# Kernel optimization log

Measured on AMD Instinct MI355X. Metric: run time of the kernel, lower is better.

Reference implementation:

```python
import jax, jax.numpy as jnp
import numpy as np


def setup_inputs() -> dict:
    key = jax.random.key(0)
    ks = jax.random.split(key, 7)
    B, P, D = 4, 2048, 1024
    s = 1.0 / np.sqrt(D)
    return {
        "x":  jax.random.normal(ks[0], (B, P, D), dtype=jnp.float32),
        "Wq": jax.random.normal(ks[1], (D, D), dtype=jnp.float32) * s,
        "bq": jnp.zeros((D,), dtype=jnp.float32),
        "Wk": jax.random.normal(ks[2], (D, D), dtype=jnp.float32) * s,
        "bk": jnp.zeros((D,), dtype=jnp.float32),
        "Wv": jax.random.normal(ks[3], (D, D), dtype=jnp.float32) * s,
        "bv": jnp.zeros((D,), dtype=jnp.float32),
    }


def reference(x, Wq, bq, Wk, bk, Wv, bv):
    # x: [B, P, D]; Linear uses W stored torch-style [out, in]: y = x @ W.T + b
    b, p, d = x.shape
    q = jnp.einsum("bpd,ed->bpe", x, Wq) + bq
    k = jnp.einsum("bpd,ed->bpe", x, Wk) + bk
    v = jnp.einsum("bpd,ed->bpe", x, Wv) + bv
    attn = jnp.einsum("bqd,bkd->bqk", q, k)  # [B, P, P]
    causal = jnp.triu(jnp.ones((p, p), dtype=bool), k=1)  # True above diagonal
    attn = jnp.where(causal, -jnp.inf, attn)
    attn = attn / jnp.sqrt(jnp.asarray(d, dtype=attn.dtype))
    scores = jax.nn.softmax(attn, axis=-1)
    # dropout is identity in eval/deterministic mode
    return jnp.einsum("bqk,bkd->bqd", scores, v)
```

## Files before the change

kernel.cpp:

```cpp
#include <hip/hip_runtime.h>
#include <hip/hip_bf16.h>


typedef __attribute__((ext_vector_type(8))) short bf16x8;
typedef __attribute__((ext_vector_type(4))) float f32x4;

__device__ __forceinline__ unsigned short f2bf(float f) {
    union { float f; unsigned u; } v; v.f = f;
    unsigned r = v.u + 0x7FFF + ((v.u >> 16) & 1);
    return (unsigned short)(r >> 16);
}

__device__ __forceinline__ void gload_lds16(const unsigned short* g, unsigned short* l) {
    __builtin_amdgcn_global_load_lds(
        (const __attribute__((address_space(1))) unsigned int*)g,
        (__attribute__((address_space(3))) unsigned int*)l, 16, 0, 0);
}

__global__ void convert_kernel(const float* __restrict__ x,  const float* __restrict__ wq,
                               const float* __restrict__ wk, const float* __restrict__ wv,
                               const float* __restrict__ bq, const float* __restrict__ bk,
                               const float* __restrict__ bv,
                               unsigned short* __restrict__ xb, unsigned short* __restrict__ wqkvb,
                               float* __restrict__ bqkv, float* __restrict__ lsum) {
    long t = (long)blockIdx.x * blockDim.x + threadIdx.x;
    long idx = t * 4;
    const float* src; unsigned short* dst; long off;
    if      (idx <  8388608) { src = x;  dst = xb;            off = idx;            }
    else if (idx <  9437184) { src = wq; dst = wqkvb;         off = idx -  8388608; }
    else if (idx < 10485760) { src = wk; dst = wqkvb+1048576; off = idx -  9437184; }
    else if (idx < 11534336) { src = wv; dst = wqkvb+2097152; off = idx - 10485760; }
    else return;
    float4 v = *(const float4*)(src + off);
    ushort4 o = make_ushort4(f2bf(v.x), f2bf(v.y), f2bf(v.z), f2bf(v.w));
    *(ushort4*)(dst + off) = o;
    if (t < 768) {
        long o2 = t * 4;
        float4 b;
        if      (o2 < 1024) b = *(const float4*)(bq + o2);
        else if (o2 < 2048) b = *(const float4*)(bk + o2 - 1024);
        else                b = *(const float4*)(bv + o2 - 2048);
        *(float4*)(bqkv + o2) = b;
    }
    if (t >= 1024 && t < 3072) {
        float4 z = make_float4(0.f, 0.f, 0.f, 0.f);
        *(float4*)(lsum + (t - 1024) * 4) = z;
    }
}

__device__ __forceinline__ void stage256(const unsigned short* gA, const unsigned short* gB,
                                         unsigned short* lds, int sdst, int t) {
    unsigned short* dst = lds + (t & 3) * 16384;
    const long koff = (long)t * 32;
    gload_lds16(gA + koff,              dst + sdst);
    gload_lds16(gA + koff + 128 * 1024, dst + 4096 + sdst);
    gload_lds16(gB + koff,              dst + 8192 + sdst);
    gload_lds16(gB + koff + 128 * 1024, dst + 12288 + sdst);
}

template<bool SWAP>
__device__ __forceinline__ void qkv256_core(const unsigned short* gA, const unsigned short* gB,
                                            unsigned short* lds, int sdst,
                                            int arow, int brow, int fch,
                                            f32x4 (&acc)[8][4]) {
    stage256(gA, gB, lds, sdst, 0);
    stage256(gA, gB, lds, sdst, 1);
    stage256(gA, gB, lds, sdst, 2);
    asm volatile("s_waitcnt vmcnt(8)" ::: "memory");
    __builtin_amdgcn_s_barrier();
#pragma unroll 1
    for (int t = 0; t < 32; ++t) {
        if (t + 3 < 32) stage256(gA, gB, lds, sdst, t + 3);
        const unsigned short* Ab = lds + (t & 3) * 16384;
        const unsigned short* Bb = Ab + 8192;
        bf16x8 af[8], bf[4];
#pragma unroll
        for (int i = 0; i < 8; ++i)
            af[i] = *(const bf16x8*)(Ab + (arow + i * 16) * 32 + fch);
#pragma unroll
        for (int j = 0; j < 4; ++j)
            bf[j] = *(const bf16x8*)(Bb + (brow + j * 16) * 32 + fch);
        __builtin_amdgcn_s_setprio(1);
#pragma unroll
        for (int i = 0; i < 8; ++i)
#pragma unroll
            for (int j = 0; j < 4; ++j)
                acc[i][j] = SWAP
                    ? __builtin_amdgcn_mfma_f32_16x16x32_bf16(bf[j], af[i], acc[i][j], 0, 0, 0)
                    : __builtin_amdgcn_mfma_f32_16x16x32_bf16(af[i], bf[j], acc[i][j], 0, 0, 0);
        __builtin_amdgcn_s_setprio(0);
        if (t <= 28)      asm volatile("s_waitcnt vmcnt(8)" ::: "memory");
        else if (t == 29) asm volatile("s_waitcnt vmcnt(4)" ::: "memory");
        else if (t == 30) asm volatile("s_waitcnt vmcnt(0)" ::: "memory");
        if (t < 31) __builtin_amdgcn_s_barrier();
    }
}

__global__ __launch_bounds__(512, 2)
void gemm_qkv256(const unsigned short* __restrict__ X,
                 const unsigned short* __restrict__ W,
                 unsigned short* __restrict__ QK,
                 unsigned short* __restrict__ VT,
                 const float* __restrict__ bias) {
    extern __shared__ unsigned short lds[];
    const int n0 = blockIdx.x * 256;
    const int m0 = blockIdx.y * 256;
    const int tid = threadIdx.x, lane = tid & 63, w = tid >> 6;
    const int q = lane >> 4, ln = lane & 15;
    const int wm = w >> 2, wn = w & 3;
    const int srow = tid >> 2;
    const int sch  = (((tid & 3) ^ ((tid >> 3) & 3)) << 3);
    const unsigned short* gA = X + (long)(m0 + srow) * 1024 + sch;
    const unsigned short* gB = W + (long)(n0 + srow) * 1024 + sch;
    const int sdst = tid * 8;
    const int arow = wm * 128 + ln;
    const int brow = wn * 64 + ln;
    const int fch  = ((q ^ ((ln >> 1) & 3)) << 3);
    f32x4 acc[8][4] = {};
    if (n0 >= 2048) {
        qkv256_core<false>(gA, gB, lds, sdst, arow, brow, fch, acc);
#pragma unroll
        for (int j = 0; j < 4; ++j) {
            const int ecol = n0 + wn * 64 + j * 16 + ln;
            const float bc = bias[ecol];
            const int e = ecol - 2048;
#pragma unroll
            for (int i = 0; i < 8; ++i) {
                const int m = m0 + wm * 128 + i * 16 + q * 4;
                ushort4 o = make_ushort4(f2bf(acc[i][j][0] + bc), f2bf(acc[i][j][1] + bc),
                                         f2bf(acc[i][j][2] + bc), f2bf(acc[i][j][3] + bc));
                *(ushort4*)(VT + (long)e * 8192 + m) = o;
            }
        }
    } else {
        qkv256_core<true>(gA, gB, lds, sdst, arow, brow, fch, acc);
#pragma unroll
        for (int j = 0; j < 4; ++j) {
            const float4 bc = *(const float4*)(bias + n0 + wn * 64 + j * 16 + q * 4);
#pragma unroll
            for (int i = 0; i < 8; ++i) {
                const int m = m0 + wm * 128 + i * 16 + ln;
                const int n = n0 + wn * 64 + j * 16 + q * 4;
                ushort4 o = make_ushort4(f2bf(acc[i][j][0] + bc.x), f2bf(acc[i][j][1] + bc.y),
                                         f2bf(acc[i][j][2] + bc.z), f2bf(acc[i][j][3] + bc.w));
                *(ushort4*)(QK + (long)m * 2048 + n) = o;
            }
        }
    }
}

__device__ __forceinline__ void stage(const unsigned short* gA, long lda,
                                      const unsigned short* gB, long ldb,
                                      unsigned short* As, unsigned short* Bs,
                                      int w, int k0) {
#pragma unroll
    for (int s = 0; s < 4; ++s) {
        gload_lds16(gA + k0 + (long)(s * 8) * lda, &As[(w * 32 + s * 8) * 64]);
        gload_lds16(gB + k0 + (long)(s * 8) * ldb, &Bs[(w * 32 + s * 8) * 64]);
    }
}

template<bool SWAP>
__device__ __forceinline__ void mfma_tile(const unsigned short* As, const unsigned short* Bs,
                                          int wr, int wc, int ln, int pr0, int pr1,
                                          f32x4 (&acc)[4][4]) {
#pragma unroll
    for (int kk = 0; kk < 2; ++kk) {
        const int pr = kk ? pr1 : pr0;
        bf16x8 af[4], bfr[4];
#pragma unroll
        for (int i = 0; i < 4; ++i)
            af[i] = *(const bf16x8*)(&As[(wr + i * 16 + ln) * 64 + pr]);
#pragma unroll
        for (int j = 0; j < 4; ++j)
            bfr[j] = *(const bf16x8*)(&Bs[(wc + j * 16 + ln) * 64 + pr]);
#pragma unroll
        for (int i = 0; i < 4; ++i)
#pragma unroll
            for (int j = 0; j < 4; ++j)
                acc[i][j] = SWAP
                    ? __builtin_amdgcn_mfma_f32_16x16x32_bf16(bfr[j], af[i], acc[i][j], 0, 0, 0)
                    : __builtin_amdgcn_mfma_f32_16x16x32_bf16(af[i], bfr[j], acc[i][j], 0, 0, 0);
    }
}

template<bool SWAP>
__device__ __forceinline__ void kloop_db(const unsigned short* gA, long lda,
                                         const unsigned short* gB, long ldb,
                                         unsigned short* As0, unsigned short* Bs0,
                                         unsigned short* As1, unsigned short* Bs1,
                                         int w, int lane, int Keff, f32x4 (&acc)[4][4]) {
    const int q  = lane >> 4;
    const int ln = lane & 15;
    const int wr = (w >> 1) * 64;
    const int wc = (w & 1) * 64;
    const int pr0 = ((q)     ^ (ln & 7)) * 8;
    const int pr1 = ((q + 4) ^ (ln & 7)) * 8;
    stage(gA, lda, gB, ldb, As0, Bs0, w, 0);
    __syncthreads();
    for (int k0 = 0; k0 < Keff; k0 += 128) {
        stage(gA, lda, gB, ldb, As1, Bs1, w, k0 + 64);
        mfma_tile<SWAP>(As0, Bs0, wr, wc, ln, pr0, pr1, acc);
        __syncthreads();
        if (k0 + 128 < Keff)
            stage(gA, lda, gB, ldb, As0, Bs0, w, k0 + 128);
        mfma_tile<SWAP>(As1, Bs1, wr, wc, ln, pr0, pr1, acc);
        __syncthreads();
    }
}

__global__ __launch_bounds__(256, 2)
void gemm_scores(const unsigned short* __restrict__ QK,
                 unsigned short* __restrict__ P,
                 float* __restrict__ lsum) {
    const int t = blockIdx.x;
    int i = (int)((sqrtf(8.0f * t + 1.0f) - 1.0f) * 0.5f);
    while ((i + 1) * (i + 2) / 2 <= t) ++i;
    while (i * (i + 1) / 2 > t) --i;
    const int j = t - i * (i + 1) / 2;
    const int m0 = i * 128, n0 = j * 128, z = blockIdx.y;
    const unsigned short* Qz = QK + (long)z * 2048 * 2048;
    const unsigned short* Kz = Qz + 1024;
    unsigned short* Pz = P + (long)z * 2048 * 2048;
    float* lz = lsum + z * 2048;

    __shared__ __align__(16) unsigned short As0[128 * 64], Bs0[128 * 64];
    __shared__ __align__(16) unsigned short As1[128 * 64], Bs1[128 * 64];
    const int tid = threadIdx.x, lane = tid & 63, w = tid >> 6;
    const int q = lane >> 4, ln = lane & 15;
    const int wr = (w >> 1) * 64, wc = (w & 1) * 64;
    const int srow = lane >> 3, sc = (lane & 7) ^ srow;
    const unsigned short* gA = Qz + (long)(m0 + w * 32 + srow) * 2048 + sc * 8;
    const unsigned short* gB = Kz + (long)(n0 + w * 32 + srow) * 2048 + sc * 8;
    f32x4 acc[4][4] = {};
    kloop_db<true>(gA, 2048, gB, 2048, As0, Bs0, As1, Bs1, w, lane, 1024, acc);

    const float scale = 0.03125f;
#pragma unroll
    for (int i2 = 0; i2 < 4; ++i2) {
        const int m = m0 + wr + i2 * 16 + ln;
        float rs = 0.f;
#pragma unroll
        for (int j2 = 0; j2 < 4; ++j2) {
            const int n = n0 + wc + j2 * 16 + q * 4;
            float p0 = (n     <= m) ? __expf(acc[i2][j2][0] * scale) : 0.f;
            float p1 = (n + 1 <= m) ? __expf(acc[i2][j2][1] * scale) : 0.f;
            float p2 = (n + 2 <= m) ? __expf(acc[i2][j2][2] * scale) : 0.f;
            float p3 = (n + 3 <= m) ? __expf(acc[i2][j2][3] * scale) : 0.f;
            rs += (p0 + p1) + (p2 + p3);
            ushort4 o = make_ushort4(f2bf(p0), f2bf(p1), f2bf(p2), f2bf(p3));
            *(ushort4*)(Pz + (long)m * 2048 + n) = o;
        }
        rs += __shfl_xor(rs, 16); rs += __shfl_xor(rs, 32);
        if (lane < 16) atomicAdd(&lz[m], rs);
    }
}

__global__ __launch_bounds__(256, 2)
void gemm_pv(const unsigned short* __restrict__ P,
             const unsigned short* __restrict__ VT,
             const float* __restrict__ lsum,
             float* __restrict__ out) {
    const int L  = blockIdx.x;
    const int ph = L >> 8;
    const int c  = L & 255;
    const int z  = c >> 6;
    const int r  = c & 63;
    const int mh = r >> 3;
    const int nt = r & 7;
    const int mt = ph ? 15 - mh : mh;
    const int m0 = mt * 128, n0 = nt * 128;
    const int Keff = m0 + 128;
    const unsigned short* Pz = P + (long)z * 2048 * 2048;
    const unsigned short* Vz = VT + (long)z * 2048;
    const float* lz = lsum + z * 2048;

    __shared__ __align__(16) unsigned short As0[128 * 64], Bs0[128 * 64];
    __shared__ __align__(16) unsigned short As1[128 * 64], Bs1[128 * 64];
    const int tid = threadIdx.x, lane = tid & 63, w = tid >> 6;
    const int q = lane >> 4, ln = lane & 15;
    const int wr = (w >> 1) * 64, wc = (w & 1) * 64;
    const int srow = lane >> 3, sc = (lane & 7) ^ srow;
    const unsigned short* gA = Pz + (long)(m0 + w * 32 + srow) * 2048 + sc * 8;
    const unsigned short* gB = Vz + (long)(n0 + w * 32 + srow) * 8192 + sc * 8;
    f32x4 acc[4][4] = {};
    kloop_db<true>(gA, 2048, gB, 8192, As0, Bs0, As1, Bs1, w, lane, Keff, acc);

#pragma unroll
    for (int i2 = 0; i2 < 4; ++i2) {
        const int m = m0 + wr + i2 * 16 + ln;
        const float inv = 1.0f / lz[m];
#pragma unroll
        for (int j2 = 0; j2 < 4; ++j2) {
            const int n = n0 + wc + j2 * 16 + q * 4;
            float4 o = make_float4(acc[i2][j2][0] * inv, acc[i2][j2][1] * inv,
                                   acc[i2][j2][2] * inv, acc[i2][j2][3] * inv);
            *(float4*)(out + (long)(z * 2048 + m) * 1024 + n) = o;
        }
    }
}

extern "C" void kernel_launch(void* const* d_in, const int* in_sizes, int n_in,
                              void* d_out, int out_size, void* d_ws, size_t ws_size,
                              hipStream_t stream) {
    const float* x  = (const float*)d_in[0];
    const float* Wq = (const float*)d_in[1];
    const float* bq = (const float*)d_in[2];
    const float* Wk = (const float*)d_in[3];
    const float* bk = (const float*)d_in[4];
    const float* Wv = (const float*)d_in[5];
    const float* bv = (const float*)d_in[6];
    float* out = (float*)d_out;

    char* ws = (char*)d_ws;
    unsigned short* xb    = (unsigned short*)ws; ws += (long)8192 * 1024 * 2;
    unsigned short* wqkvb = (unsigned short*)ws; ws += (long)3072 * 1024 * 2;
    float*          bqkv  = (float*)ws;          ws += (long)3072 * 4;
    float*          lsum  = (float*)ws;          ws += (long)8192 * 4;
    unsigned short* QKb   = (unsigned short*)ws; ws += (long)8192 * 2048 * 2;
    unsigned short* VTb   = (unsigned short*)ws; ws += (long)1024 * 8192 * 2;
    unsigned short* Pb    = (unsigned short*)ws; ws += (long)4 * 2048 * 2048 * 2;

    hipFuncSetAttribute((const void*)gemm_qkv256,
                        hipFuncAttributeMaxDynamicSharedMemorySize, 131072);

    hipLaunchKernelGGL(convert_kernel, dim3(11264), dim3(256), 0, stream,
                       x, Wq, Wk, Wv, bq, bk, bv, xb, wqkvb, bqkv, lsum);

    hipLaunchKernelGGL(gemm_qkv256, dim3(12, 32, 1), dim3(512), 131072, stream,
                       xb, wqkvb, QKb, VTb, bqkv);

    hipLaunchKernelGGL(gemm_scores, dim3(136, 4, 1), dim3(256), 0, stream,
                       QKb, Pb, lsum);

    hipLaunchKernelGGL(gemm_pv, dim3(512, 1, 1), dim3(256), 0, stream,
                       Pb, VTb, lsum, out);
}
```

Measured before the change: 252.7 us.

## Restructure QKV GEMM main loop into 8-phase interleaved load/MFMA pipeline with BK=64

Rewrites the 256x256 QKV projection GEMM core so each K step covers 64 elements in two double-buffered halves. Global-to-LDS loads for the next tiles are spread across eight MFMA phases separated by barriers, with a wider 8-chunk XOR swizzle for the new row width. The goal is to hide memory latency and LDS reads behind MFMA work with finer-grained overlap. The cost is many more barriers per iteration and tighter register and LDS scheduling.

```diff
diff --git a/kernel.cpp b/kernel.cpp
--- a/kernel.cpp
+++ b/kernel.cpp
@@ -48,51 +48,119 @@
     }
 }
 
-__device__ __forceinline__ void stage256(const unsigned short* gA, const unsigned short* gB,
-                                         unsigned short* lds, int sdst, int t) {
-    unsigned short* dst = lds + (t & 3) * 16384;
-    const long koff = (long)t * 32;
-    gload_lds16(gA + koff,              dst + sdst);
-    gload_lds16(gA + koff + 128 * 1024, dst + 4096 + sdst);
-    gload_lds16(gB + koff,              dst + 8192 + sdst);
-    gload_lds16(gB + koff + 128 * 1024, dst + 12288 + sdst);
-}
+__device__ __forceinline__ void stage_half(const unsigned short* gth, unsigned short* ldst) {
+    gload_lds16(gth,             ldst);
+    gload_lds16(gth + 64 * 1024, ldst + 4096);
+}
+
+template<bool SWAP, int I0, int J0>
+__device__ __forceinline__ void mfma16(bf16x8 (&af)[4][2], bf16x8 (&bf)[4][2],
+                                       f32x4 (&acc)[8][4]) {
+#pragma unroll
+    for (int i = 0; i < 4; ++i)
+#pragma unroll
+        for (int j = 0; j < 2; ++j)
+#pragma unroll
+            for (int kk = 0; kk < 2; ++kk) {
+                f32x4& a = acc[I0 + i][J0 + j];
+                a = SWAP
+                    ? __builtin_amdgcn_mfma_f32_16x16x32_bf16(bf[J0 + j][kk], af[i][kk], a, 0, 0, 0)
+                    : __builtin_amdgcn_mfma_f32_16x16x32_bf16(af[i][kk], bf[J0 + j][kk], a, 0, 0, 0);
+            }
+}
+
+__device__ __forceinline__ void read_af(const unsigned short* Ah, int ih, int rA0, int rA1,
+                                        bf16x8 (&af)[4][2]) {
+#pragma unroll
+    for (int i = 0; i < 4; ++i) {
+        af[i][0] = *(const bf16x8*)(Ah + (ih * 4 + i) * 1024 + rA0);
+        af[i][1] = *(const bf16x8*)(Ah + (ih * 4 + i) * 1024 + rA1);
+    }
+}
+__device__ __forceinline__ void read_bf(const unsigned short* Bh, int rB0, int rB1,
+                                        bf16x8 (&bf)[4][2]) {
+#pragma unroll
+    for (int j = 0; j < 4; ++j) {
+        bf[j][0] = *(const bf16x8*)(Bh + j * 1024 + rB0);
+        bf[j][1] = *(const bf16x8*)(Bh + j * 1024 + rB1);
+    }
+}
+
+#define SBAR __builtin_amdgcn_s_barrier()
+#define PRIO1 __builtin_amdgcn_s_setprio(1)
+#define PRIO0 __builtin_amdgcn_s_setprio(0)
 
 template<bool SWAP>
-__device__ __forceinline__ void qkv256_core(const unsigned short* gA, const unsigned short* gB,
-                                            unsigned short* lds, int sdst,
-                                            int arow, int brow, int fch,
-                                            f32x4 (&acc)[8][4]) {
-    stage256(gA, gB, lds, sdst, 0);
-    stage256(gA, gB, lds, sdst, 1);
-    stage256(gA, gB, lds, sdst, 2);
-    asm volatile("s_waitcnt vmcnt(8)" ::: "memory");
-    __builtin_amdgcn_s_barrier();
+__device__ __forceinline__ void qkv8p_core(const unsigned short* aTh, const unsigned short* bTh,
+                                           unsigned short* lds, int tid,
+                                           int wm, int wn, int q, int ln,
+                                           f32x4 (&acc)[8][4]) {
+    const int rA0 = ln * 64 + ((q)     ^ (ln & 7)) * 8;
+    const int rA1 = ln * 64 + ((q + 4) ^ (ln & 7)) * 8;
+    const int rB0 = (wn & 1) * 4096 + rA0;
+    const int rB1 = (wn & 1) * 4096 + rA1;
+    unsigned short* sd = lds + tid * 8;
+    const unsigned short* Ah0 = lds +         wm * 8192;
+    const unsigned short* Bh0 = lds + 16384 + (wn >> 1) * 8192;
+    const unsigned short* Ah1 = Ah0 + 32768;
+    const unsigned short* Bh1 = Bh0 + 32768;
+    bf16x8 af[4][2], bf[4][2];
+
+    stage_half(aTh,               sd + 0);
+    stage_half(aTh + 131072,      sd + 8192);
+    stage_half(bTh,               sd + 16384);
+    stage_half(bTh + 131072,      sd + 24576);
+    stage_half(bTh + 64,          sd + 32768 + 16384);
+    stage_half(bTh + 131072 + 64, sd + 32768 + 24576);
+    stage_half(aTh + 64,          sd + 32768 + 0);
+    asm volatile("s_waitcnt vmcnt(6)" ::: "memory");
+    SBAR;
+
 #pragma unroll 1
-    for (int t = 0; t < 32; ++t) {
-        if (t + 3 < 32) stage256(gA, gB, lds, sdst, t + 3);
-        const unsigned short* Ab = lds + (t & 3) * 16384;
-        const unsigned short* Bb = Ab + 8192;
-        bf16x8 af[8], bf[4];
-#pragma unroll
-        for (int i = 0; i < 8; ++i)
-            af[i] = *(const bf16x8*)(Ab + (arow + i * 16) * 32 + fch);
-#pragma unroll
-        for (int j = 0; j < 4; ++j)
-            bf[j] = *(const bf16x8*)(Bb + (brow + j * 16) * 32 + fch);
-        __builtin_amdgcn_s_setprio(1);
-#pragma unroll
-        for (int i = 0; i < 8; ++i)
-#pragma unroll
-            for (int j = 0; j < 4; ++j)
-                acc[i][j] = SWAP
-                    ? __builtin_amdgcn_mfma_f32_16x16x32_bf16(bf[j], af[i], acc[i][j], 0, 0, 0)
-                    : __builtin_amdgcn_mfma_f32_16x16x32_bf16(af[i], bf[j], acc[i][j], 0, 0, 0);
-        __builtin_amdgcn_s_setprio(0);
-        if (t <= 28)      asm volatile("s_waitcnt vmcnt(8)" ::: "memory");
-        else if (t == 29) asm volatile("s_waitcnt vmcnt(4)" ::: "memory");
-        else if (t == 30) asm volatile("s_waitcnt vmcnt(0)" ::: "memory");
-        if (t < 31) __builtin_amdgcn_s_barrier();
+    for (int it = 0; it < 8; ++it) {
+        const int k0 = it * 128;
+        const bool pf = (it < 7);
+        read_af(Ah0, 0, rA0, rA1, af);
+        read_bf(Bh0, rB0, rB1, bf);
+        stage_half(aTh + 131072 + (k0 + 64), sd + 32768 + 8192);
+        SBAR;
+        PRIO1; mfma16<SWAP, 0, 0>(af, bf, acc); PRIO0;
+        SBAR;
+        if (pf) stage_half(bTh + (k0 + 128), sd + 16384);
+        SBAR;
+        PRIO1; mfma16<SWAP, 0, 2>(af, bf, acc); PRIO0;
+        SBAR;
+        read_af(Ah0, 1, rA0, rA1, af);
+        if (pf) stage_half(bTh + 131072 + (k0 + 128), sd + 24576);
+        SBAR;
+        PRIO1; mfma16<SWAP, 4, 0>(af, bf, acc); PRIO0;
+        SBAR;
+        if (pf) stage_half(aTh + (k0 + 128), sd + 0);
+        SBAR;
+        PRIO1; mfma16<SWAP, 4, 2>(af, bf, acc); PRIO0;
+        if (pf) { asm volatile("s_waitcnt vmcnt(6)" ::: "memory"); }
+        else    { asm volatile("s_waitcnt vmcnt(0)" ::: "memory"); }
+        SBAR;
+        read_af(Ah1, 0, rA0, rA1, af);
+        read_bf(Bh1, rB0, rB1, bf);
+        if (pf) stage_half(aTh + 131072 + (k0 + 128), sd + 8192);
+        SBAR;
+        PRIO1; mfma16<SWAP, 0, 0>(af, bf, acc); PRIO0;
+        SBAR;
+        if (pf) stage_half(bTh + (k0 + 192), sd + 32768 + 16384);
+        SBAR;
+        PRIO1; mfma16<SWAP, 0, 2>(af, bf, acc); PRIO0;
+        SBAR;
+        read_af(Ah1, 1, rA0, rA1, af);
+        if (pf) stage_half(bTh + 131072 + (k0 + 192), sd + 32768 + 24576);
+        SBAR;
+        PRIO1; mfma16<SWAP, 4, 0>(af, bf, acc); PRIO0;
+        SBAR;
+        if (pf) stage_half(aTh + (k0 + 192), sd + 32768 + 0);
+        SBAR;
+        PRIO1; mfma16<SWAP, 4, 2>(af, bf, acc); PRIO0;
+        asm volatile("s_waitcnt vmcnt(6)" ::: "memory");
+        SBAR;
     }
 }
 
@@ -108,17 +176,13 @@
     const int tid = threadIdx.x, lane = tid & 63, w = tid >> 6;
     const int q = lane >> 4, ln = lane & 15;
     const int wm = w >> 2, wn = w & 3;
-    const int srow = tid >> 2;
-    const int sch  = (((tid & 3) ^ ((tid >> 3) & 3)) << 3);
-    const unsigned short* gA = X + (long)(m0 + srow) * 1024 + sch;
-    const unsigned short* gB = W + (long)(n0 + srow) * 1024 + sch;
-    const int sdst = tid * 8;
-    const int arow = wm * 128 + ln;
-    const int brow = wn * 64 + ln;
-    const int fch  = ((q ^ ((ln >> 1) & 3)) << 3);
+    const int srow = tid >> 3;
+    const int sch  = (((tid & 7) ^ (srow & 7)) << 3);
+    const unsigned short* aTh = X + (long)(m0 + srow) * 1024 + sch;
+    const unsigned short* bTh = W + (long)(n0 + srow) * 1024 + sch;
     f32x4 acc[8][4] = {};
     if (n0 >= 2048) {
-        qkv256_core<false>(gA, gB, lds, sdst, arow, brow, fch, acc);
+        qkv8p_core<false>(aTh, bTh, lds, tid, wm, wn, q, ln, acc);
 #pragma unroll
         for (int j = 0; j < 4; ++j) {
             const int ecol = n0 + wn * 64 + j * 16 + ln;
@@ -133,7 +197,7 @@
             }
         }
     } else {
-        qkv256_core<true>(gA, gB, lds, sdst, arow, brow, fch, acc);
+        qkv8p_core<true>(aTh, bTh, lds, tid, wm, wn, q, ln, acc);
 #pragma unroll
         for (int j = 0; j < 4; ++j) {
             const float4 bc = *(const float4*)(bias + n0 + wn * 64 + j * 16 + q * 4);
```

Measured after the change: 248.0 us. About the same (-1.8%).
